# Kernel tuning notes

Hardware: AMD Instinct MI355X
Metric: run time of the kernel (lower is better)

The kernel has to match this reference:

```python
import jax, jax.numpy as jnp
import numpy as np
import math

D_MODEL = 1024
N_HEADS = 16
D_K = D_MODEL // N_HEADS
BS, SQ, SK = 2, 2048, 2048


def setup_inputs() -> dict:
    key = jax.random.key(0)
    ks = jax.random.split(key, 7)
    q = jax.random.normal(ks[0], (BS, SQ, D_MODEL), dtype=jnp.float32)
    k = jax.random.normal(ks[1], (BS, SK, D_MODEL), dtype=jnp.float32)
    v = jax.random.normal(ks[2], (BS, SK, D_MODEL), dtype=jnp.float32)
    # causal mask: True = masked out (matches torch masked_fill semantics)
    mask = jnp.broadcast_to(
        ~jnp.tril(jnp.ones((SQ, SK), dtype=bool)), (BS, SQ, SK))
    scale = 1.0 / math.sqrt(D_MODEL)
    wq = jax.random.normal(ks[3], (D_MODEL, D_MODEL), dtype=jnp.float32) * scale
    wk = jax.random.normal(ks[4], (D_MODEL, D_MODEL), dtype=jnp.float32) * scale
    wv = jax.random.normal(ks[5], (D_MODEL, D_MODEL), dtype=jnp.float32) * scale
    wo = jax.random.normal(ks[6], (D_MODEL, D_MODEL), dtype=jnp.float32) * scale
    return {"q": q, "k": k, "v": v, "mask": mask,
            "wq": wq, "wk": wk, "wv": wv, "wo": wo}


def reference(q, k, v, mask, wq, wk, wv, wo):
    bs, sq, _ = q.shape
    sk = k.shape[1]
    # nn.Linear(bias=False): x @ W.T ; reshape to heads -> [b, h, s, d_k]
    qh = (q @ wq.T).reshape(bs, sq, N_HEADS, D_K).transpose(0, 2, 1, 3)
    kh = (k @ wk.T).reshape(bs, sk, N_HEADS, D_K).transpose(0, 2, 1, 3)
    vh = (v @ wv.T).reshape(bs, sk, N_HEADS, D_K).transpose(0, 2, 1, 3)
    # scaled dot-product attention, full [b,h,sq,sk] scores (as original)
    z = jnp.einsum('bhqd,bhkd->bhqk', qh, kh) / math.sqrt(D_K)
    z = jnp.where(mask[:, None, :, :], jnp.float32(-1e10), z)
    z = jax.nn.softmax(z, axis=-1)
    z = jnp.einsum('bhqk,bhkd->bhqd', z, vh)
    z = z.transpose(0, 2, 1, 3).reshape(bs, sq, D_MODEL)
    return z @ wo.T
```

## Files before the change

### kernel.cpp

```cpp
#include <hip/hip_runtime.h>
#include <hip/hip_bf16.h>
#include <stdint.h>

typedef short s16x8 __attribute__((ext_vector_type(8)));
typedef float f32x4 __attribute__((ext_vector_type(4)));

#define BSZ 2
#define SQL 2048
#define DMODEL 1024
#define NHEAD 16
#define DKH 64

#if __has_builtin(__builtin_amdgcn_exp2f)
#define EXP2(x) __builtin_amdgcn_exp2f(x)
#else
#define EXP2(x) exp2f(x)
#endif

__device__ __forceinline__ ushort f2bf(float f) {
  uint32_t u = __float_as_uint(f);
  u += 0x7fffu + ((u >> 16) & 1u);
  return (ushort)(u >> 16);
}

__device__ __forceinline__ uint32_t cvtpk_bf16(float lo, float hi) {
  uint32_t r;
  asm("v_cvt_pk_bf16_f32 %0, %1, %2" : "=v"(r) : "v"(lo), "v"(hi));
  return r;
}

__device__ __forceinline__ float rowmax16(float x) {
  x = fmaxf(x, __int_as_float(__builtin_amdgcn_update_dpp(0, __float_as_int(x), 0x121, 0xf, 0xf, true)));
  x = fmaxf(x, __int_as_float(__builtin_amdgcn_update_dpp(0, __float_as_int(x), 0x122, 0xf, 0xf, true)));
  x = fmaxf(x, __int_as_float(__builtin_amdgcn_update_dpp(0, __float_as_int(x), 0x124, 0xf, 0xf, true)));
  x = fmaxf(x, __int_as_float(__builtin_amdgcn_update_dpp(0, __float_as_int(x), 0x128, 0xf, 0xf, true)));
  return x;
}

__device__ __forceinline__ void gload_lds16(const ushort* g, ushort* l) {
  __builtin_amdgcn_global_load_lds((const __attribute__((address_space(1))) void*)g,
                                   (__attribute__((address_space(3))) void*)l,
                                   16, 0, 0);
}

__global__ void cvt_all(const float* __restrict__ q, const float* __restrict__ k,
                        const float* __restrict__ v, const float* __restrict__ wq,
                        const float* __restrict__ wk, const float* __restrict__ wv,
                        const float* __restrict__ wo, ushort* __restrict__ dq,
                        ushort* __restrict__ dk, ushort* __restrict__ dv,
                        ushort* __restrict__ dwq, ushort* __restrict__ dwk,
                        ushort* __restrict__ dwv, ushort* __restrict__ dwo) {
  int b = blockIdx.x;
  const float* s; ushort* d; int off;
  if (b < 4096)       { s = q;  d = dq;  off = b; }
  else if (b < 8192)  { s = k;  d = dk;  off = b - 4096; }
  else if (b < 12288) { s = v;  d = dv;  off = b - 8192; }
  else if (b < 13312) { s = wq; d = dwq; off = b - 12288; }
  else if (b < 14336) { s = wk; d = dwk; off = b - 13312; }
  else if (b < 15360) { s = wv; d = dwv; off = b - 14336; }
  else                { s = wo; d = dwo; off = b - 15360; }
  int i = (off * 256 + threadIdx.x) * 4;
  float4 x = *(const float4*)(s + i);
  ushort4 o;
  o.x = f2bf(x.x); o.y = f2bf(x.y); o.z = f2bf(x.z); o.w = f2bf(x.w);
  *(ushort4*)(d + i) = o;
}

__device__ __forceinline__ void gemm_core(const ushort* __restrict__ A,
                                          const ushort* __restrict__ B,
                                          ushort* sA, ushort* sB, f32x4 (&acc)[4][4]) {
  const int t = threadIdx.x, w = t >> 6, lane = t & 63;
  const int lrow = lane & 15, lk = (lane >> 4) * 8;
  const int m0 = blockIdx.x * 128, n0 = blockIdx.y * 128;
  const int wm = (w >> 1) * 64, wn = (w & 1) * 64;

  auto stage = [&](int kt, int buf) {
#pragma unroll
    for (int i = 0; i < 2; ++i) {
      int ci = i * 256 + t;
      int row = ci >> 2;
      int ce = (ci & 3) * 8;
      gload_lds16(A + (size_t)(m0 + row) * 1024 + kt * 32 + ce,
                  sA + buf * 4096 + (i * 256 + w * 64) * 8);
      gload_lds16(B + (size_t)(n0 + row) * 1024 + kt * 32 + ce,
                  sB + buf * 4096 + (i * 256 + w * 64) * 8);
    }
  };

  stage(0, 0);
  for (int kt = 0; kt < 32; ++kt) {
    const int cur = kt & 1;
    if (kt < 31) {
      stage(kt + 1, cur ^ 1);
      asm volatile("s_waitcnt vmcnt(4)" ::: "memory");
    } else {
      asm volatile("s_waitcnt vmcnt(0)" ::: "memory");
    }
    __builtin_amdgcn_s_barrier();
    __builtin_amdgcn_sched_barrier(0);
    const ushort* pA = sA + cur * 4096;
    const ushort* pB = sB + cur * 4096;
    s16x8 af[4], bfr[4];
#pragma unroll
    for (int mi = 0; mi < 4; ++mi)
      af[mi] = *(const s16x8*)(pA + (wm + mi * 16 + lrow) * 32 + lk);
#pragma unroll
    for (int ni = 0; ni < 4; ++ni)
      bfr[ni] = *(const s16x8*)(pB + (wn + ni * 16 + lrow) * 32 + lk);
    __builtin_amdgcn_s_setprio(1);
#pragma unroll
    for (int mi = 0; mi < 4; ++mi)
#pragma unroll
      for (int ni = 0; ni < 4; ++ni)
        acc[mi][ni] = __builtin_amdgcn_mfma_f32_16x16x32_bf16(af[mi], bfr[ni], acc[mi][ni], 0, 0, 0);
    __builtin_amdgcn_s_setprio(0);
    asm volatile("s_waitcnt lgkmcnt(0)" ::: "memory");
    __builtin_amdgcn_s_barrier();
  }
}

__device__ __forceinline__ void epi_heads(f32x4 (&acc)[4][4], ushort* D, float scale, bool vtrans) {
  const int lane = threadIdx.x & 63, w = threadIdx.x >> 6;
  const int m0 = blockIdx.x * 128, n0 = blockIdx.y * 128;
  const int wm = (w >> 1) * 64, wn = (w & 1) * 64;
#pragma unroll
  for (int mi = 0; mi < 4; ++mi)
#pragma unroll
    for (int ni = 0; ni < 4; ++ni)
#pragma unroll
      for (int r = 0; r < 4; ++r) {
        int m = m0 + wm + mi * 16 + (lane >> 4) * 4 + r;
        int n = n0 + wn + ni * 16 + (lane & 15);
        ushort bv = f2bf(acc[mi][ni][r] * scale);
        int b = m >> 11, s = m & 2047, h = n >> 6, d = n & 63;
        if (vtrans)
          D[((size_t)((b * 16 + h) * 64 + d)) * 2048 + s] = bv;
        else
          D[((size_t)((b * 16 + h) * 2048 + s)) * 64 + d] = bv;
      }
}

__global__ __launch_bounds__(256) void gemm_qkv(const ushort* __restrict__ qb,
                                                const ushort* __restrict__ kb,
                                                const ushort* __restrict__ vb,
                                                const ushort* __restrict__ wqb,
                                                const ushort* __restrict__ wkb,
                                                const ushort* __restrict__ wvb,
                                                ushort* __restrict__ Qh,
                                                ushort* __restrict__ Kh,
                                                ushort* __restrict__ Vt) {
  __shared__ __align__(16) ushort sA[2 * 128 * 32];
  __shared__ __align__(16) ushort sB[2 * 128 * 32];
  const int z = blockIdx.z;
  const ushort* A = (z == 0) ? qb : (z == 1) ? kb : vb;
  const ushort* B = (z == 0) ? wqb : (z == 1) ? wkb : wvb;
  f32x4 acc[4][4] = {};
  gemm_core(A, B, sA, sB, acc);
  ushort* D = (z == 0) ? Qh : (z == 1) ? Kh : Vt;
  epi_heads(acc, D, (z == 0) ? 0.18033688f : 1.0f, z == 2);
}

__global__ __launch_bounds__(256) void gemm_out(const ushort* __restrict__ A,
                                                const ushort* __restrict__ B,
                                                float* __restrict__ D) {
  __shared__ __align__(16) ushort sA[2 * 128 * 32];
  __shared__ __align__(16) ushort sB[2 * 128 * 32];
  f32x4 acc[4][4] = {};
  gemm_core(A, B, sA, sB, acc);
  const int lane = threadIdx.x & 63, w = threadIdx.x >> 6;
  const int m0 = blockIdx.x * 128, n0 = blockIdx.y * 128;
  const int wm = (w >> 1) * 64, wn = (w & 1) * 64;
#pragma unroll
  for (int mi = 0; mi < 4; ++mi)
#pragma unroll
    for (int ni = 0; ni < 4; ++ni)
#pragma unroll
      for (int r = 0; r < 4; ++r) {
        int m = m0 + wm + mi * 16 + (lane >> 4) * 4 + r;
        int n = n0 + wn + ni * 16 + (lane & 15);
        D[(size_t)m * 1024 + n] = acc[mi][ni][r];
      }
}

__global__ __launch_bounds__(512) void attn_fwd(const ushort* __restrict__ Qh,
                                                const ushort* __restrict__ Kh,
                                                const ushort* __restrict__ Vt,
                                                ushort* __restrict__ Z) {
  __shared__ __align__(16) ushort sK[2][64 * 64];
  __shared__ __align__(16) ushort sV[2][64 * 64];
  __shared__ __align__(16) ushort sP[8][16 * 72];
  const int t = threadIdx.x, w = t >> 6, lane = t & 63;
  const int lcol = lane & 15, lhi = lane >> 4;
  const int p = blockIdx.x, bh = blockIdx.y;
  const int qlo = p, qhi = 31 - p;
  const int setid = w >> 2;
  const int qtile = setid ? qhi : qlo;
  const int qr0 = qtile * 64 + (w & 3) * 16;
  const ushort* Qb = Qh + (size_t)bh * SQL * DKH;
  const ushort* Kb = Kh + (size_t)bh * SQL * DKH;
  const ushort* Vb = Vt + (size_t)bh * DKH * SQL;

  s16x8 qf0, qf1;
  {
    const ushort* qp = Qb + (size_t)(qr0 + lcol) * DKH + lhi * 8;
    qf0 = *(const s16x8*)qp;
    qf1 = *(const s16x8*)(qp + 32);
  }
  float mr[4], lrp[4];
  f32x4 o[4] = {};
#pragma unroll
  for (int r = 0; r < 4; ++r) { mr[r] = -1e30f; lrp[r] = 0.f; }
  ushort* Pw = &sP[w][0];

  auto stage = [&](int kb, int buf) {
    int row = t >> 3, cc = t & 7;
    int scz = cc ^ (row & 7);
    gload_lds16(Kb + (size_t)(kb * 64 + row) * DKH + scz * 8, &sK[buf][w * 512]);
    gload_lds16(Vb + (size_t)row * SQL + kb * 64 + scz * 8, &sV[buf][w * 512]);
  };

  const int nkb = qhi + 1;
  stage(0, 0);
  for (int kb = 0; kb < nkb; ++kb) {
    const int cur = kb & 1;
    if (kb + 1 < nkb) {
      stage(kb + 1, cur ^ 1);
      asm volatile("s_waitcnt vmcnt(2)" ::: "memory");
    } else {
      asm volatile("s_waitcnt vmcnt(0)" ::: "memory");
    }
    __builtin_amdgcn_s_barrier();
    __builtin_amdgcn_sched_barrier(0);
    const bool act = setid || (kb <= qlo);
    if (act) {
      const ushort* pK = &sK[cur][0];
      const ushort* pV = &sV[cur][0];
      f32x4 sc4[4];
      __builtin_amdgcn_s_setprio(1);
#pragma unroll
      for (int ktt = 0; ktt < 4; ++ktt) {
        int row = ktt * 16 + lcol;
        int c0 = lhi ^ (row & 7);
        int c1 = (lhi + 4) ^ (row & 7);
        s16x8 k0 = *(const s16x8*)(pK + row * 64 + c0 * 8);
        s16x8 k1 = *(const s16x8*)(pK + row * 64 + c1 * 8);
        f32x4 a = {};
        a = __builtin_amdgcn_mfma_f32_16x16x32_bf16(qf0, k0, a, 0, 0, 0);
        a = __builtin_amdgcn_mfma_f32_16x16x32_bf16(qf1, k1, a, 0, 0, 0);
        sc4[ktt] = a;
      }
      __builtin_amdgcn_s_setprio(0);
      if (kb == qtile) {
#pragma unroll
        for (int ktt = 0; ktt < 4; ++ktt) {
          int kloc = ktt * 16 + lcol;
#pragma unroll
          for (int r = 0; r < 4; ++r)
            if (kloc > (w & 3) * 16 + lhi * 4 + r) sc4[ktt][r] = -1e30f;
        }
      }
      float tm4[4];
#pragma unroll
      for (int r = 0; r < 4; ++r) {
        float tm = fmaxf(fmaxf(sc4[0][r], sc4[1][r]), fmaxf(sc4[2][r], sc4[3][r]));
        tm4[r] = rowmax16(tm);
      }
      bool grow = (tm4[0] > mr[0] + 8.f) || (tm4[1] > mr[1] + 8.f) ||
                  (tm4[2] > mr[2] + 8.f) || (tm4[3] > mr[3] + 8.f);
      if (__any((int)grow)) {
#pragma unroll
        for (int r = 0; r < 4; ++r) {
          float mn = fmaxf(mr[r], tm4[r]);
          float al = EXP2(mr[r] - mn);
          lrp[r] *= al;
          o[0][r] *= al; o[1][r] *= al; o[2][r] *= al; o[3][r] *= al;
          mr[r] = mn;
        }
      }
#pragma unroll
      for (int r = 0; r < 4; ++r) {
        float p0 = EXP2(sc4[0][r] - mr[r]);
        float p1 = EXP2(sc4[1][r] - mr[r]);
        float p2 = EXP2(sc4[2][r] - mr[r]);
        float p3 = EXP2(sc4[3][r] - mr[r]);
        lrp[r] += (p0 + p1) + (p2 + p3);
        uint32_t w01 = cvtpk_bf16(p0, p1);
        uint32_t w23 = cvtpk_bf16(p2, p3);
        ushort* pr = Pw + (lhi * 4 + r) * 72 + lcol;
        pr[0]  = (ushort)(w01 & 0xffffu);
        pr[16] = (ushort)(w01 >> 16);
        pr[32] = (ushort)(w23 & 0xffffu);
        pr[48] = (ushort)(w23 >> 16);
      }
      __builtin_amdgcn_s_setprio(1);
#pragma unroll
      for (int kc = 0; kc < 2; ++kc) {
        s16x8 pf = *(const s16x8*)(Pw + lcol * 72 + kc * 32 + lhi * 8);
#pragma unroll
        for (int dt = 0; dt < 4; ++dt) {
          int row = dt * 16 + lcol;
          int cc = (lhi + 4 * kc) ^ (row & 7);
          s16x8 vf = *(const s16x8*)(pV + row * 64 + cc * 8);
          o[dt] = __builtin_amdgcn_mfma_f32_16x16x32_bf16(pf, vf, o[dt], 0, 0, 0);
        }
      }
      __builtin_amdgcn_s_setprio(0);
    }
    asm volatile("s_waitcnt lgkmcnt(0)" ::: "memory");
    __builtin_amdgcn_s_barrier();
  }

  const int b = bh >> 4, h = bh & 15;
#pragma unroll
  for (int r = 0; r < 4; ++r) {
    float sum = lrp[r];
    sum += __shfl_xor(sum, 1);
    sum += __shfl_xor(sum, 2);
    sum += __shfl_xor(sum, 4);
    sum += __shfl_xor(sum, 8);
    float inv = 1.0f / sum;
    int q = qr0 + lhi * 4 + r;
    size_t base = ((size_t)(b * SQL + q)) * DMODEL + h * DKH + lcol;
#pragma unroll
    for (int dt = 0; dt < 4; ++dt)
      Z[base + dt * 16] = f2bf(o[dt][r] * inv);
  }
}

extern "C" void kernel_launch(void* const* d_in, const int* in_sizes, int n_in,
                              void* d_out, int out_size, void* d_ws, size_t ws_size,
                              hipStream_t stream) {
  const float* q = (const float*)d_in[0];
  const float* k = (const float*)d_in[1];
  const float* v = (const float*)d_in[2];
  const float* wq = (const float*)d_in[4];
  const float* wk = (const float*)d_in[5];
  const float* wv = (const float*)d_in[6];
  const float* wo = (const float*)d_in[7];

  const size_t NBIG = (size_t)BSZ * SQL * DMODEL;
  const size_t NW = (size_t)DMODEL * DMODEL;
  ushort* qb = (ushort*)d_ws;
  ushort* kb = qb + NBIG;
  ushort* vb = kb + NBIG;
  ushort* wqb = vb + NBIG;
  ushort* wkb = wqb + NW;
  ushort* wvb = wkb + NW;
  ushort* wob = wvb + NW;
  ushort* Qh = wob + NW;
  ushort* Kh = Qh + NBIG;
  ushort* Vt = Kh + NBIG;
  ushort* Z  = Vt + NBIG;

  cvt_all<<<dim3(16384), 256, 0, stream>>>(q, k, v, wq, wk, wv, wo,
                                           qb, kb, vb, wqb, wkb, wvb, wob);
  gemm_qkv<<<dim3(32, 8, 3), 256, 0, stream>>>(qb, kb, vb, wqb, wkb, wvb, Qh, Kh, Vt);
  attn_fwd<<<dim3(16, BSZ * NHEAD), 512, 0, stream>>>(Qh, Kh, Vt, Z);
  gemm_out<<<dim3(32, 8), 256, 0, stream>>>(Z, wob, (float*)d_out);
}
```

Measured before the change: 132.0 us.

## Use k-major LDS layout in GEMMs, permute V columns, 64-row output GEMM

Changes the GEMM shared-memory staging to a k-chunk-major layout so each lane's fragment read is contiguous and conflict-free. It also permutes the sequence index in the transposed V so the attention kernel can write P with one packed 8-byte store instead of four scalar stores. The output projection moves to 64x128 tiles, doubling its block count for better CU occupancy. The cost is extra index arithmetic and a tight coupling between the V permutation and the P layout.

```diff
diff --git a/kernel.cpp b/kernel.cpp
--- a/kernel.cpp
+++ b/kernel.cpp
@@ -70,7 +70,7 @@
                                           const ushort* __restrict__ B,
                                           ushort* sA, ushort* sB, f32x4 (&acc)[4][4]) {
   const int t = threadIdx.x, w = t >> 6, lane = t & 63;
-  const int lrow = lane & 15, lk = (lane >> 4) * 8;
+  const int lrow = lane & 15, g = lane >> 4;
   const int m0 = blockIdx.x * 128, n0 = blockIdx.y * 128;
   const int wm = (w >> 1) * 64, wn = (w & 1) * 64;
 
@@ -78,11 +78,10 @@
 #pragma unroll
     for (int i = 0; i < 2; ++i) {
       int ci = i * 256 + t;
-      int row = ci >> 2;
-      int ce = (ci & 3) * 8;
-      gload_lds16(A + (size_t)(m0 + row) * 1024 + kt * 32 + ce,
+      int r = ci & 127, c = ci >> 7;
+      gload_lds16(A + (size_t)(m0 + r) * 1024 + kt * 32 + c * 8,
                   sA + buf * 4096 + (i * 256 + w * 64) * 8);
-      gload_lds16(B + (size_t)(n0 + row) * 1024 + kt * 32 + ce,
+      gload_lds16(B + (size_t)(n0 + r) * 1024 + kt * 32 + c * 8,
                   sB + buf * 4096 + (i * 256 + w * 64) * 8);
     }
   };
@@ -103,10 +102,10 @@
     s16x8 af[4], bfr[4];
 #pragma unroll
     for (int mi = 0; mi < 4; ++mi)
-      af[mi] = *(const s16x8*)(pA + (wm + mi * 16 + lrow) * 32 + lk);
+      af[mi] = *(const s16x8*)(pA + g * 1024 + (wm + mi * 16 + lrow) * 8);
 #pragma unroll
     for (int ni = 0; ni < 4; ++ni)
-      bfr[ni] = *(const s16x8*)(pB + (wn + ni * 16 + lrow) * 32 + lk);
+      bfr[ni] = *(const s16x8*)(pB + g * 1024 + (wn + ni * 16 + lrow) * 8);
     __builtin_amdgcn_s_setprio(1);
 #pragma unroll
     for (int mi = 0; mi < 4; ++mi)
@@ -133,10 +132,12 @@
         int n = n0 + wn + ni * 16 + (lane & 15);
         ushort bv = f2bf(acc[mi][ni][r] * scale);
         int b = m >> 11, s = m & 2047, h = n >> 6, d = n & 63;
-        if (vtrans)
-          D[((size_t)((b * 16 + h) * 64 + d)) * 2048 + s] = bv;
-        else
+        if (vtrans) {
+          int sp = (s & ~63) | (((s & 15) << 2) | ((s >> 4) & 3));
+          D[((size_t)((b * 16 + h) * 64 + d)) * 2048 + sp] = bv;
+        } else {
           D[((size_t)((b * 16 + h) * 2048 + s)) * 64 + d] = bv;
+        }
       }
 }
 
@@ -149,8 +150,8 @@
                                                 ushort* __restrict__ Qh,
                                                 ushort* __restrict__ Kh,
                                                 ushort* __restrict__ Vt) {
-  __shared__ __align__(16) ushort sA[2 * 128 * 32];
-  __shared__ __align__(16) ushort sB[2 * 128 * 32];
+  __shared__ __align__(16) ushort sA[2 * 4096];
+  __shared__ __align__(16) ushort sB[2 * 4096];
   const int z = blockIdx.z;
   const ushort* A = (z == 0) ? qb : (z == 1) ? kb : vb;
   const ushort* B = (z == 0) ? wqb : (z == 1) ? wkb : wvb;
@@ -160,18 +161,65 @@
   epi_heads(acc, D, (z == 0) ? 0.18033688f : 1.0f, z == 2);
 }
 
-__global__ __launch_bounds__(256) void gemm_out(const ushort* __restrict__ A,
-                                                const ushort* __restrict__ B,
-                                                float* __restrict__ D) {
-  __shared__ __align__(16) ushort sA[2 * 128 * 32];
-  __shared__ __align__(16) ushort sB[2 * 128 * 32];
-  f32x4 acc[4][4] = {};
-  gemm_core(A, B, sA, sB, acc);
-  const int lane = threadIdx.x & 63, w = threadIdx.x >> 6;
-  const int m0 = blockIdx.x * 128, n0 = blockIdx.y * 128;
-  const int wm = (w >> 1) * 64, wn = (w & 1) * 64;
-#pragma unroll
-  for (int mi = 0; mi < 4; ++mi)
+__global__ __launch_bounds__(256) void gemm_out64(const ushort* __restrict__ A,
+                                                  const ushort* __restrict__ B,
+                                                  float* __restrict__ D) {
+  __shared__ __align__(16) ushort sA[2 * 2048];
+  __shared__ __align__(16) ushort sB[2 * 4096];
+  const int t = threadIdx.x, w = t >> 6, lane = t & 63;
+  const int lrow = lane & 15, g = lane >> 4;
+  const int m0 = blockIdx.x * 64, n0 = blockIdx.y * 128;
+  const int wm = (w >> 1) * 32, wn = (w & 1) * 64;
+  f32x4 acc[2][4] = {};
+
+  auto stage = [&](int kt, int buf) {
+    {
+      int r = t & 63, c = t >> 6;
+      gload_lds16(A + (size_t)(m0 + r) * 1024 + kt * 32 + c * 8,
+                  sA + buf * 2048 + (w * 64) * 8);
+    }
+#pragma unroll
+    for (int i = 0; i < 2; ++i) {
+      int ci = i * 256 + t;
+      int r = ci & 127, c = ci >> 7;
+      gload_lds16(B + (size_t)(n0 + r) * 1024 + kt * 32 + c * 8,
+                  sB + buf * 4096 + (i * 256 + w * 64) * 8);
+    }
+  };
+
+  stage(0, 0);
+  for (int kt = 0; kt < 32; ++kt) {
+    const int cur = kt & 1;
+    if (kt < 31) {
+      stage(kt + 1, cur ^ 1);
+      asm volatile("s_waitcnt vmcnt(3)" ::: "memory");
+    } else {
+      asm volatile("s_waitcnt vmcnt(0)" ::: "memory");
+    }
+    __builtin_amdgcn_s_barrier();
+    __builtin_amdgcn_sched_barrier(0);
+    const ushort* pA = sA + cur * 2048;
+    const ushort* pB = sB + cur * 4096;
+    s16x8 af[2], bfr[4];
+#pragma unroll
+    for (int mi = 0; mi < 2; ++mi)
+      af[mi] = *(const s16x8*)(pA + g * 512 + (wm + mi * 16 + lrow) * 8);
+#pragma unroll
+    for (int ni = 0; ni < 4; ++ni)
+      bfr[ni] = *(const s16x8*)(pB + g * 1024 + (wn + ni * 16 + lrow) * 8);
+    __builtin_amdgcn_s_setprio(1);
+#pragma unroll
+    for (int mi = 0; mi < 2; ++mi)
+#pragma unroll
+      for (int ni = 0; ni < 4; ++ni)
+        acc[mi][ni] = __builtin_amdgcn_mfma_f32_16x16x32_bf16(af[mi], bfr[ni], acc[mi][ni], 0, 0, 0);
+    __builtin_amdgcn_s_setprio(0);
+    asm volatile("s_waitcnt lgkmcnt(0)" ::: "memory");
+    __builtin_amdgcn_s_barrier();
+  }
+
+#pragma unroll
+  for (int mi = 0; mi < 2; ++mi)
 #pragma unroll
     for (int ni = 0; ni < 4; ++ni)
 #pragma unroll
@@ -284,13 +332,10 @@
         float p2 = EXP2(sc4[2][r] - mr[r]);
         float p3 = EXP2(sc4[3][r] - mr[r]);
         lrp[r] += (p0 + p1) + (p2 + p3);
-        uint32_t w01 = cvtpk_bf16(p0, p1);
-        uint32_t w23 = cvtpk_bf16(p2, p3);
-        ushort* pr = Pw + (lhi * 4 + r) * 72 + lcol;
-        pr[0]  = (ushort)(w01 & 0xffffu);
-        pr[16] = (ushort)(w01 >> 16);
-        pr[32] = (ushort)(w23 & 0xffffu);
-        pr[48] = (ushort)(w23 >> 16);
+        uint2 pk;
+        pk.x = cvtpk_bf16(p0, p1);
+        pk.y = cvtpk_bf16(p2, p3);
+        *(uint2*)(Pw + (lhi * 4 + r) * 72 + lcol * 4) = pk;
       }
       __builtin_amdgcn_s_setprio(1);
 #pragma unroll
@@ -356,5 +401,5 @@
                                            qb, kb, vb, wqb, wkb, wvb, wob);
   gemm_qkv<<<dim3(32, 8, 3), 256, 0, stream>>>(qb, kb, vb, wqb, wkb, wvb, Qh, Kh, Vt);
   attn_fwd<<<dim3(16, BSZ * NHEAD), 512, 0, stream>>>(Qh, Kh, Vt, Z);
-  gemm_out<<<dim3(32, 8), 256, 0, stream>>>(Z, wob, (float*)d_out);
-}
+  gemm_out64<<<dim3(64, 8), 256, 0, stream>>>(Z, wob, (float*)d_out);
+}
```

After: 161.3 us. +22.2%, slower.
